# Kernel optimization log

Hardware: AMD Instinct MI355X
Metric: run time of the kernel (lower is better)

## Reference

```python
import jax, jax.numpy as jnp
import numpy as np

H = 16           # attn_num
ROPE_THETA = 10000.0

def _rope(x):
    # x: [B, H, S, A]; non-interleaved (rotate-half) RoPE matching RotaryEmb
    A = x.shape[-1]
    S = x.shape[2]
    inv_freq = (1.0 / ROPE_THETA) ** (jnp.arange(0, A, 2, dtype=jnp.float32) / A)  # [A/2]
    t = jnp.arange(S, dtype=jnp.float32)
    freqs = t[:, None] * inv_freq[None, :]            # [S, A/2]
    cos = jnp.cos(freqs)[None, None, :, :]
    sin = jnp.sin(freqs)[None, None, :, :]
    x1, x2 = jnp.split(x, 2, axis=-1)
    y1 = x1 * cos + x2 * sin
    y2 = -x1 * sin + x2 * cos
    return jnp.concatenate([y1, y2], axis=-1).astype(x.dtype)

def setup_inputs() -> dict:
    key = jax.random.key(0)
    kq, kk, kv = jax.random.split(key, 3)
    B, S, D = 2, 2048, 2048
    return {
        "xq": jax.random.normal(kq, (B, S, D), dtype=jnp.float32),
        "xk": jax.random.normal(kk, (B, S, D), dtype=jnp.float32),
        "xv": jax.random.normal(kv, (B, S, D), dtype=jnp.float32),
    }

def reference(xq, xk, xv):
    B, S, D = xq.shape
    A = D // H
    # b s (h a) -> b h s a
    q = xq.reshape(B, S, H, A).transpose(0, 2, 1, 3)
    k = xk.reshape(B, S, H, A).transpose(0, 2, 1, 3)
    v = xv.reshape(B, S, H, A).transpose(0, 2, 1, 3)
    q = _rope(q)
    k = _rope(k)
    scale = 1.0 / jnp.sqrt(jnp.asarray(A, dtype=q.dtype))
    scores = jnp.einsum('bhsa,bhta->bhst', q, k) * scale   # [B,H,S,S]
    causal = jnp.tril(jnp.ones((S, S), dtype=bool))
    scores = jnp.where(causal[None, None, :, :], scores, jnp.asarray(-jnp.inf, scores.dtype))
    probs = jax.nn.softmax(scores, axis=-1)
    out = jnp.einsum('bhst,bhta->bhsa', probs, v)          # [B,H,S,A]
    # b h s a -> b s (h a)
    return out.transpose(0, 2, 1, 3).reshape(B, S, D)
```

## Files before the change

kernel.cpp:

```cpp
#include <hip/hip_runtime.h>
#include <stdint.h>

#define H_HEADS 16
#define ADIM    128
#define SLEN    2048
#define DMODEL  2048

typedef __attribute__((ext_vector_type(8))) short  short8;
typedef __attribute__((ext_vector_type(4))) float  float4v;
typedef __attribute__((ext_vector_type(4))) unsigned short ushort4v;

typedef const __attribute__((address_space(1))) unsigned int gas_u32;
typedef __attribute__((address_space(3))) unsigned int las_u32;

union F4 { float4 v; float a[4]; };
union PU { unsigned u[4]; short8 s; };

__device__ __forceinline__ unsigned short f2bf(float f) {
  union { float f; unsigned u; } v; v.f = f;
  unsigned r = v.u + 0x7FFFu + ((v.u >> 16) & 1u);
  return (unsigned short)(r >> 16);
}
__device__ __forceinline__ unsigned cvt_pk_bf16(float lo, float hi) {
  unsigned r;
  asm("v_cvt_pk_bf16_f32 %0, %1, %2" : "=v"(r) : "v"(lo), "v"(hi));
  return r;
}
__device__ __forceinline__ void xswap(unsigned& a, unsigned& b) {
  asm volatile("v_permlane32_swap_b32 %0, %1" : "+v"(a), "+v"(b));
  asm volatile("v_permlane16_swap_b32 %0, %1" : "+v"(a), "+v"(b));
}
__device__ __forceinline__ float fsin01(float r) { float o; asm("v_sin_f32 %0, %1" : "=v"(o) : "v"(r)); return o; }
__device__ __forceinline__ float fcos01(float r) { float o; asm("v_cos_f32 %0, %1" : "=v"(o) : "v"(r)); return o; }
__device__ __forceinline__ float ffract(float x) { float o; asm("v_fract_f32 %0, %1" : "=v"(o) : "v"(x)); return o; }
__device__ __forceinline__ float hexp2(float x)  { float o; asm("v_exp_f32 %0, %1" : "=v"(o) : "v"(x)); return o; }

#define ROPE_C 0.20762050593045935f
#define L2I2PI -2.651496129472319f
#define C2LOG  0.12751879523103988f
#define Z0     8.0f

__global__ __launch_bounds__(256) void prep_k(const float* __restrict__ xk,
                                              unsigned short* __restrict__ kw) {
  int t = blockIdx.x * 256 + threadIdx.x;
  int i4 = t & 15;
  int h  = (t >> 4) & (H_HEADS - 1);
  int s  = (t >> 8) & (SLEN - 1);
  int b  = t >> 19;
  int i0 = i4 * 4;
  long ib = ((long)(b * SLEN + s)) * DMODEL + h * ADIM;
  F4 x1, x2;
  x1.v = *(const float4*)(xk + ib + i0);
  x2.v = *(const float4*)(xk + ib + i0 + 64);
  ushort4v o1, o2;
  #pragma unroll
  for (int j = 0; j < 4; ++j) {
    float rev = (float)s * exp2f(fmaf(-(float)(i0 + j), ROPE_C, L2I2PI));
    float r = ffract(rev);
    float sn = fsin01(r), cs = fcos01(r);
    o1[j] = f2bf( x1.a[j] * cs + x2.a[j] * sn);
    o2[j] = f2bf(-x1.a[j] * sn + x2.a[j] * cs);
  }
  long row = ((long)((b * H_HEADS + h) * SLEN + s)) * ADIM;
  int swz = s & 7;
  int c1 = ((((i0     ) >> 3) ^ swz) << 3) | (i0 & 7);
  int c2 = ((((i0 + 64) >> 3) ^ swz) << 3) | (i0 & 7);
  *(ushort4v*)(kw + row + c1) = o1;
  *(ushort4v*)(kw + row + c2) = o2;
}

__global__ __launch_bounds__(256) void prep_v(const float* __restrict__ xv,
                                              unsigned short* __restrict__ vw) {
  __shared__ float lv[32 * 129];
  int jt = blockIdx.x;
  int bh = blockIdx.y;
  int b = bh >> 4, h = bh & (H_HEADS - 1);
  int t = threadIdx.x;
  #pragma unroll
  for (int it = 0; it < 4; ++it) {
    int id  = it * 256 + t;
    int row = id >> 5;
    int c4  = (id & 31) * 4;
    F4 x;
    x.v = *(const float4*)(xv + ((long)(b * SLEN + jt * 32 + row)) * DMODEL + h * ADIM + c4);
    #pragma unroll
    for (int jj = 0; jj < 4; ++jj) lv[row * 129 + c4 + jj] = x.a[jj];
  }
  __syncthreads();
  unsigned short* vt = vw + ((long)(bh * 64 + jt)) * 4096;
  #pragma unroll
  for (int it = 0; it < 4; ++it) {
    int id = it * 256 + t;
    int d  = id >> 3;
    int i  = id & 7;
    ushort4v o;
    #pragma unroll
    for (int jj = 0; jj < 4; ++jj) o[jj] = f2bf(lv[(4 * i + jj) * 129 + d]);
    *(ushort4v*)(vt + d * 32 + i * 4) = o;
  }
}

__global__ __launch_bounds__(256, 3) void attn_fwd(const float* __restrict__ xq,
                                                   const unsigned short* __restrict__ kw,
                                                   const unsigned short* __restrict__ vw,
                                                   float* __restrict__ out) {
  __shared__ __align__(16) unsigned char sbuf[36864];
  unsigned short* kB = (unsigned short*)sbuf;
  float4v* mergeO = (float4v*)sbuf;
  float4v* mergeL = (float4v*)(sbuf + 32768);

  int n = blockIdx.x;
  int xcd = n & 7, j = n >> 3;
  int bh = xcd * 4 + (j & 3);
  int c  = 31 - (j >> 2);
  int b = bh >> 4, h = bh & (H_HEADS - 1);
  int t = threadIdx.x, l = t & 63, w = t >> 6;
  int wq = w >> 1, g = w & 1;
  int lq = l & 15, gq = l >> 4, lq7 = lq & 7;
  int basew = c * 64 + wq * 32;
  int sq0 = basew + lq, sq1 = basew + 16 + lq;

  short8 qf0[4], qf1[4];
  auto ROPEQ = [&](int sq, short8 (&qf)[4]) {
    const float* qsrc = xq + ((long)(b * SLEN + sq)) * DMODEL + h * ADIM;
    float q32[4][8];
    #pragma unroll
    for (int cc = 0; cc < 4; ++cc) {
      F4 lo, hi;
      lo.v = *(const float4*)(qsrc + cc * 32 + gq * 8);
      hi.v = *(const float4*)(qsrc + cc * 32 + gq * 8 + 4);
      #pragma unroll
      for (int jj = 0; jj < 4; ++jj) { q32[cc][jj] = lo.a[jj]; q32[cc][jj + 4] = hi.a[jj]; }
    }
    #pragma unroll
    for (int cc = 0; cc < 2; ++cc) {
      #pragma unroll
      for (int jj = 0; jj < 8; ++jj) {
        int a = cc * 32 + gq * 8 + jj;
        float rev = (float)sq * exp2f(fmaf(-(float)a, ROPE_C, L2I2PI));
        float r = ffract(rev);
        float sn = fsin01(r), cs = fcos01(r);
        qf[cc    ][jj] = (short)f2bf( q32[cc][jj] * cs + q32[cc + 2][jj] * sn);
        qf[cc + 2][jj] = (short)f2bf(-q32[cc][jj] * sn + q32[cc + 2][jj] * cs);
      }
    }
  };
  ROPEQ(sq0, qf0);
  ROPEQ(sq1, qf1);

  float4v acc0[8], acc1[8], lacc0, lacc1;
  #pragma unroll
  for (int i = 0; i < 8; ++i) { acc0[i] = (float4v){0.f,0.f,0.f,0.f}; acc1[i] = (float4v){0.f,0.f,0.f,0.f}; }
  lacc0 = (float4v){0.f,0.f,0.f,0.f};
  lacc1 = (float4v){0.f,0.f,0.f,0.f};
  const float4v Z4 = (float4v){0.f,0.f,0.f,0.f};

  PU ones;
  ones.u[0] = 0x3F803F80u; ones.u[1] = 0x3F803F80u; ones.u[2] = 0x3F803F80u; ones.u[3] = 0x3F803F80u;

  const unsigned short* kbase = kw + (long)bh * SLEN * ADIM;
  const unsigned short* vbase = vw + (long)bh * 64 * 4096;

  unsigned short* kst[2] = { kB + (g * 2 + 0) * 4096, kB + (g * 2 + 1) * 4096 };
  const unsigned short* klr[2] = { kst[0] + lq * 128, kst[1] + lq * 128 };
  int koff[4];
  #pragma unroll
  for (int cc = 0; cc < 4; ++cc) koff[cc] = ((cc * 4 + gq) ^ lq7) << 3;
  int vlane = lq * 32 + gq * 8;

  auto STAGE = [&](unsigned short* kd, int tile) {
    const unsigned short* ks = kbase + (long)tile * 4096;
    #pragma unroll
    for (int i = 0; i < 4; ++i) {
      int seg = wq * 4 + i;
      __builtin_amdgcn_global_load_lds((gas_u32*)(ks + seg * 512 + l * 8),
                                       (las_u32*)&kd[seg * 512], 16, 0, 0);
    }
  };

  auto SMAX = [&](float4v (&sv)[2], int sq, bool dg, int tj, float4v& lac) -> short8 {
    float p[8];
    #pragma unroll
    for (int kb = 0; kb < 2; ++kb) {
      #pragma unroll
      for (int r = 0; r < 4; ++r) {
        float e = fmaf(sv[kb][r], C2LOG, -Z0);
        if (dg && (tj * 32 + kb * 16 + gq * 4 + r > sq)) e = -1e30f;
        p[kb * 4 + r] = hexp2(e);
      }
    }
    unsigned L0 = cvt_pk_bf16(p[0], p[1]);
    unsigned H0 = cvt_pk_bf16(p[2], p[3]);
    unsigned L1 = cvt_pk_bf16(p[4], p[5]);
    unsigned H1 = cvt_pk_bf16(p[6], p[7]);
    xswap(L0, L1);
    xswap(H0, H1);
    PU a;
    a.u[0] = L0; a.u[1] = H0; a.u[2] = L1; a.u[3] = H1;
    lac = __builtin_amdgcn_mfma_f32_16x16x32_bf16(a.s, ones.s, lac, 0, 0, 0);
    return a.s;
  };

  int M = c + 1;

  auto ITER = [&](int m, const unsigned short* klrow, unsigned short* kn) {
    if (m + 1 < M) STAGE(kn, 2 * (m + 1) + g);
    int tj = 2 * m + g;
    bool act = (tj * 32 <= basew + 31);
    if (act) {
      const unsigned short* vt = vbase + (long)tj * 4096;
      short8 vbA[4];
      #pragma unroll
      for (int db = 0; db < 4; ++db)
        vbA[db] = *(const short8*)(vt + db * 512 + vlane);

      float4v s0[2], s1[2];
      __builtin_amdgcn_s_setprio(1);
      {
        #pragma unroll
        for (int kb = 0; kb < 2; ++kb) {
          short8 kf = *(const short8*)&klrow[kb * 2048 + koff[0]];
          s0[kb] = __builtin_amdgcn_mfma_f32_16x16x32_bf16(kf, qf0[0], Z4, 0, 0, 0);
          s1[kb] = __builtin_amdgcn_mfma_f32_16x16x32_bf16(kf, qf1[0], Z4, 0, 0, 0);
        }
        #pragma unroll
        for (int cc = 1; cc < 4; ++cc) {
          #pragma unroll
          for (int kb = 0; kb < 2; ++kb) {
            short8 kf = *(const short8*)&klrow[kb * 2048 + koff[cc]];
            s0[kb] = __builtin_amdgcn_mfma_f32_16x16x32_bf16(kf, qf0[cc], s0[kb], 0, 0, 0);
            s1[kb] = __builtin_amdgcn_mfma_f32_16x16x32_bf16(kf, qf1[cc], s1[kb], 0, 0, 0);
          }
        }
      }
      __builtin_amdgcn_s_setprio(0);

      bool dg = (tj * 32 + 31 > basew);
      short8 pa0 = SMAX(s0, sq0, dg, tj, lacc0);
      short8 pa1 = SMAX(s1, sq1, dg, tj, lacc1);

      short8 vbB[4];
      #pragma unroll
      for (int db = 0; db < 4; ++db)
        vbB[db] = *(const short8*)(vt + (db + 4) * 512 + vlane);

      __builtin_amdgcn_s_setprio(1);
      #pragma unroll
      for (int db = 0; db < 4; ++db) {
        acc0[db] = __builtin_amdgcn_mfma_f32_16x16x32_bf16(pa0, vbA[db], acc0[db], 0, 0, 0);
        acc1[db] = __builtin_amdgcn_mfma_f32_16x16x32_bf16(pa1, vbA[db], acc1[db], 0, 0, 0);
      }
      #pragma unroll
      for (int db = 0; db < 4; ++db) {
        acc0[db + 4] = __builtin_amdgcn_mfma_f32_16x16x32_bf16(pa0, vbB[db], acc0[db + 4], 0, 0, 0);
        acc1[db + 4] = __builtin_amdgcn_mfma_f32_16x16x32_bf16(pa1, vbB[db], acc1[db + 4], 0, 0, 0);
      }
      __builtin_amdgcn_s_setprio(0);
    }
    asm volatile("s_waitcnt vmcnt(0)" ::: "memory");
    __builtin_amdgcn_s_barrier();
  };

  STAGE(kst[0], g);
  asm volatile("s_waitcnt vmcnt(0)" ::: "memory");
  __builtin_amdgcn_s_barrier();

  int m = 0;
  for (; m + 2 <= M; m += 2) {
    ITER(m,     klr[0], kst[1]);
    ITER(m + 1, klr[1], kst[0]);
  }
  if (m < M) ITER(m, klr[0], kst[1]);

  if (g == 1) {
    float4v* dst = mergeO + wq * 1024;
    #pragma unroll
    for (int i = 0; i < 8; ++i) {
      dst[i * 64 + l]       = acc0[i];
      dst[(8 + i) * 64 + l] = acc1[i];
    }
    float4v* ld = mergeL + wq * 128;
    ld[l]      = lacc0;
    ld[64 + l] = lacc1;
  }
  __builtin_amdgcn_s_barrier();

  if (g == 0) {
    const float4v* src = mergeO + wq * 1024;
    #pragma unroll
    for (int i = 0; i < 8; ++i) {
      float4v b0 = src[i * 64 + l];
      float4v b1 = src[(8 + i) * 64 + l];
      #pragma unroll
      for (int r = 0; r < 4; ++r) { acc0[i][r] += b0[r]; acc1[i][r] += b1[r]; }
    }
    const float4v* ls = mergeL + wq * 128;
    float4v lb0 = ls[l], lb1 = ls[64 + l];
    #pragma unroll
    for (int r = 0; r < 4; ++r) { lacc0[r] += lb0[r]; lacc1[r] += lb1[r]; }

    auto EPI = [&](int base, float4v& lac, float4v (&acc)[8]) {
      float linv[4];
      #pragma unroll
      for (int r = 0; r < 4; ++r) linv[r] = 1.0f / lac[r];
      #pragma unroll
      for (int db = 0; db < 8; ++db)
        #pragma unroll
        for (int r = 0; r < 4; ++r)
          out[((long)(b * SLEN + base + gq * 4 + r)) * DMODEL + h * ADIM + db * 16 + lq]
            = acc[db][r] * linv[r];
    };
    EPI(basew,      lacc0, acc0);
    EPI(basew + 16, lacc1, acc1);
  }
}

extern "C" void kernel_launch(void* const* d_in, const int* in_sizes, int n_in,
                              void* d_out, int out_size, void* d_ws, size_t ws_size,
                              hipStream_t stream) {
  const float* xq = (const float*)d_in[0];
  const float* xk = (const float*)d_in[1];
  const float* xv = (const float*)d_in[2];
  float* outp = (float*)d_out;
  int B = in_sizes[0] / (SLEN * DMODEL);
  size_t perT = (size_t)B * H_HEADS * SLEN * ADIM;
  unsigned short* kw = (unsigned short*)d_ws;
  unsigned short* vw = kw + perT;

  prep_k<<<dim3(B * 2048), 256, 0, stream>>>(xk, kw);
  prep_v<<<dim3(64, B * H_HEADS), 256, 0, stream>>>(xv, vw);
  attn_fwd<<<dim3(B * H_HEADS * 32), 256, 0, stream>>>(xq, kw, vw, outp);
}
```

Measured before the change: 90.35 us.

## Use 128-row query tiles with shared K/V LDS staging and swizzled V

Each block now covers 128 query rows, one 32-row slice per wave, instead of 64 rows split across two key-interleaved wave groups. K and V tiles are double-buffered in LDS through async global-to-LDS loads and shared by all four waves, so the cross-wave partial-sum merge is no longer needed. The V layout written by prep_v is XOR-swizzled so the LDS reads avoid bank conflicts. The grid is halved and blocks are ordered so heavy and light causal tiles are paired. The trade-off is fewer blocks (512) and causal imbalance across the waves inside a block, since idle waves still wait at every barrier.

```diff
diff --git a/kernel.cpp b/kernel.cpp
--- a/kernel.cpp
+++ b/kernel.cpp
@@ -96,7 +96,8 @@
     ushort4v o;
     #pragma unroll
     for (int jj = 0; jj < 4; ++jj) o[jj] = f2bf(lv[(4 * i + jj) * 129 + d]);
-    *(ushort4v*)(vt + d * 32 + i * 4) = o;
+    int ch = ((i >> 1) ^ (d & 3) ^ ((d >> 2) & 3));
+    *(ushort4v*)(vt + d * 32 + (ch << 3) + ((i & 1) << 2)) = o;
   }
 }
 
@@ -104,20 +105,18 @@
                                                    const unsigned short* __restrict__ kw,
                                                    const unsigned short* __restrict__ vw,
                                                    float* __restrict__ out) {
-  __shared__ __align__(16) unsigned char sbuf[36864];
-  unsigned short* kB = (unsigned short*)sbuf;
-  float4v* mergeO = (float4v*)sbuf;
-  float4v* mergeL = (float4v*)(sbuf + 32768);
+  __shared__ __align__(16) unsigned short kL[2][32 * 128];
+  __shared__ __align__(16) unsigned short vL[2][128 * 32];
 
   int n = blockIdx.x;
-  int xcd = n & 7, j = n >> 3;
-  int bh = xcd * 4 + (j & 3);
-  int c  = 31 - (j >> 2);
+  int xcd = n & 7;
+  int j   = (n < 256) ? (n >> 3) : ((n - 256) >> 3);
+  int bh  = xcd * 4 + (j & 3);
+  int c   = (n < 256) ? (15 - (j >> 2)) : (j >> 2);
   int b = bh >> 4, h = bh & (H_HEADS - 1);
   int t = threadIdx.x, l = t & 63, w = t >> 6;
-  int wq = w >> 1, g = w & 1;
-  int lq = l & 15, gq = l >> 4, lq7 = lq & 7;
-  int basew = c * 64 + wq * 32;
+  int lq = l & 15, gq = l >> 4, lq7 = lq & 7, lq3 = lq & 3;
+  int basew = c * 128 + w * 32;
   int sq0 = basew + lq, sq1 = basew + 16 + lq;
 
   short8 qf0[4], qf1[4];
@@ -161,20 +160,25 @@
   const unsigned short* kbase = kw + (long)bh * SLEN * ADIM;
   const unsigned short* vbase = vw + (long)bh * 64 * 4096;
 
-  unsigned short* kst[2] = { kB + (g * 2 + 0) * 4096, kB + (g * 2 + 1) * 4096 };
+  unsigned short* kst[2] = { &kL[0][0], &kL[1][0] };
+  unsigned short* vst[2] = { &vL[0][0], &vL[1][0] };
   const unsigned short* klr[2] = { kst[0] + lq * 128, kst[1] + lq * 128 };
+  const unsigned short* vlr[2] = { vst[0] + lq * 32 + ((gq ^ lq3 ^ (lq >> 2)) << 3),
+                                   vst[1] + lq * 32 + ((gq ^ lq3 ^ (lq >> 2)) << 3) };
   int koff[4];
   #pragma unroll
   for (int cc = 0; cc < 4; ++cc) koff[cc] = ((cc * 4 + gq) ^ lq7) << 3;
-  int vlane = lq * 32 + gq * 8;
-
-  auto STAGE = [&](unsigned short* kd, int tile) {
+
+  auto STAGE = [&](unsigned short* kd, unsigned short* vd, int tile) {
     const unsigned short* ks = kbase + (long)tile * 4096;
-    #pragma unroll
-    for (int i = 0; i < 4; ++i) {
-      int seg = wq * 4 + i;
+    const unsigned short* vs = vbase + (long)tile * 4096;
+    #pragma unroll
+    for (int i = 0; i < 2; ++i) {
+      int seg = w * 2 + i;
       __builtin_amdgcn_global_load_lds((gas_u32*)(ks + seg * 512 + l * 8),
                                        (las_u32*)&kd[seg * 512], 16, 0, 0);
+      __builtin_amdgcn_global_load_lds((gas_u32*)(vs + seg * 512 + l * 8),
+                                       (las_u32*)&vd[seg * 512], 16, 0, 0);
     }
   };
 
@@ -201,19 +205,13 @@
     return a.s;
   };
 
-  int M = c + 1;
-
-  auto ITER = [&](int m, const unsigned short* klrow, unsigned short* kn) {
-    if (m + 1 < M) STAGE(kn, 2 * (m + 1) + g);
-    int tj = 2 * m + g;
-    bool act = (tj * 32 <= basew + 31);
+  int nt = 4 * c + 4;
+
+  auto ITER = [&](int m, const unsigned short* klrow, const unsigned short* vlrow,
+                  unsigned short* kn, unsigned short* vn) {
+    if (m + 1 < nt) STAGE(kn, vn, m + 1);
+    bool act = (m <= 4 * c + w);
     if (act) {
-      const unsigned short* vt = vbase + (long)tj * 4096;
-      short8 vbA[4];
-      #pragma unroll
-      for (int db = 0; db < 4; ++db)
-        vbA[db] = *(const short8*)(vt + db * 512 + vlane);
-
       float4v s0[2], s1[2];
       __builtin_amdgcn_s_setprio(1);
       {
@@ -235,25 +233,16 @@
       }
       __builtin_amdgcn_s_setprio(0);
 
-      bool dg = (tj * 32 + 31 > basew);
-      short8 pa0 = SMAX(s0, sq0, dg, tj, lacc0);
-      short8 pa1 = SMAX(s1, sq1, dg, tj, lacc1);
-
-      short8 vbB[4];
-      #pragma unroll
-      for (int db = 0; db < 4; ++db)
-        vbB[db] = *(const short8*)(vt + (db + 4) * 512 + vlane);
+      bool dg = (m * 32 + 31 > basew);
+      short8 pa0 = SMAX(s0, sq0, dg, m, lacc0);
+      short8 pa1 = SMAX(s1, sq1, dg, m, lacc1);
 
       __builtin_amdgcn_s_setprio(1);
       #pragma unroll
-      for (int db = 0; db < 4; ++db) {
-        acc0[db] = __builtin_amdgcn_mfma_f32_16x16x32_bf16(pa0, vbA[db], acc0[db], 0, 0, 0);
-        acc1[db] = __builtin_amdgcn_mfma_f32_16x16x32_bf16(pa1, vbA[db], acc1[db], 0, 0, 0);
-      }
-      #pragma unroll
-      for (int db = 0; db < 4; ++db) {
-        acc0[db + 4] = __builtin_amdgcn_mfma_f32_16x16x32_bf16(pa0, vbB[db], acc0[db + 4], 0, 0, 0);
-        acc1[db + 4] = __builtin_amdgcn_mfma_f32_16x16x32_bf16(pa1, vbB[db], acc1[db + 4], 0, 0, 0);
+      for (int db = 0; db < 8; ++db) {
+        short8 vb = *(const short8*)&vlrow[db * 512];
+        acc0[db] = __builtin_amdgcn_mfma_f32_16x16x32_bf16(pa0, vb, acc0[db], 0, 0, 0);
+        acc1[db] = __builtin_amdgcn_mfma_f32_16x16x32_bf16(pa1, vb, acc1[db], 0, 0, 0);
       }
       __builtin_amdgcn_s_setprio(0);
     }
@@ -261,58 +250,28 @@
     __builtin_amdgcn_s_barrier();
   };
 
-  STAGE(kst[0], g);
+  STAGE(kst[0], vst[0], 0);
   asm volatile("s_waitcnt vmcnt(0)" ::: "memory");
   __builtin_amdgcn_s_barrier();
 
-  int m = 0;
-  for (; m + 2 <= M; m += 2) {
-    ITER(m,     klr[0], kst[1]);
-    ITER(m + 1, klr[1], kst[0]);
-  }
-  if (m < M) ITER(m, klr[0], kst[1]);
-
-  if (g == 1) {
-    float4v* dst = mergeO + wq * 1024;
-    #pragma unroll
-    for (int i = 0; i < 8; ++i) {
-      dst[i * 64 + l]       = acc0[i];
-      dst[(8 + i) * 64 + l] = acc1[i];
-    }
-    float4v* ld = mergeL + wq * 128;
-    ld[l]      = lacc0;
-    ld[64 + l] = lacc1;
-  }
-  __builtin_amdgcn_s_barrier();
-
-  if (g == 0) {
-    const float4v* src = mergeO + wq * 1024;
-    #pragma unroll
-    for (int i = 0; i < 8; ++i) {
-      float4v b0 = src[i * 64 + l];
-      float4v b1 = src[(8 + i) * 64 + l];
-      #pragma unroll
-      for (int r = 0; r < 4; ++r) { acc0[i][r] += b0[r]; acc1[i][r] += b1[r]; }
-    }
-    const float4v* ls = mergeL + wq * 128;
-    float4v lb0 = ls[l], lb1 = ls[64 + l];
-    #pragma unroll
-    for (int r = 0; r < 4; ++r) { lacc0[r] += lb0[r]; lacc1[r] += lb1[r]; }
-
-    auto EPI = [&](int base, float4v& lac, float4v (&acc)[8]) {
-      float linv[4];
-      #pragma unroll
-      for (int r = 0; r < 4; ++r) linv[r] = 1.0f / lac[r];
-      #pragma unroll
-      for (int db = 0; db < 8; ++db)
-        #pragma unroll
-        for (int r = 0; r < 4; ++r)
-          out[((long)(b * SLEN + base + gq * 4 + r)) * DMODEL + h * ADIM + db * 16 + lq]
-            = acc[db][r] * linv[r];
-    };
-    EPI(basew,      lacc0, acc0);
-    EPI(basew + 16, lacc1, acc1);
-  }
+  for (int m = 0; m < nt; m += 2) {
+    ITER(m,     klr[0], vlr[0], kst[1], vst[1]);
+    ITER(m + 1, klr[1], vlr[1], kst[0], vst[0]);
+  }
+
+  auto EPI = [&](int base, float4v& lac, float4v (&acc)[8]) {
+    float linv[4];
+    #pragma unroll
+    for (int r = 0; r < 4; ++r) linv[r] = 1.0f / lac[r];
+    #pragma unroll
+    for (int db = 0; db < 8; ++db)
+      #pragma unroll
+      for (int r = 0; r < 4; ++r)
+        out[((long)(b * SLEN + base + gq * 4 + r)) * DMODEL + h * ADIM + db * 16 + lq]
+          = acc[db][r] * linv[r];
+  };
+  EPI(basew,      lacc0, acc0);
+  EPI(basew + 16, lacc1, acc1);
 }
 
 extern "C" void kernel_launch(void* const* d_in, const int* in_sizes, int n_in,
@@ -329,5 +288,5 @@
 
   prep_k<<<dim3(B * 2048), 256, 0, stream>>>(xk, kw);
   prep_v<<<dim3(64, B * H_HEADS), 256, 0, stream>>>(xv, vw);
-  attn_fwd<<<dim3(B * H_HEADS * 32), 256, 0, stream>>>(xq, kw, vw, outp);
-}
+  attn_fwd<<<dim3(B * H_HEADS * 16), 256, 0, stream>>>(xq, kw, vw, outp);
+}
```

New measurement: 93.86 us. 1.04x slower.
